# Kernel tuning notes

Measured on AMD Instinct MI355X. Metric: run time of the kernel, lower is better.

The kernel has to match this reference:

```python
import jax, jax.numpy as jnp
import numpy as np

B, C, N = 8, 512, 2048

def setup_inputs() -> dict:
    key = jax.random.key(0)
    ks = jax.random.split(key, 7)
    s = 1.0 / np.sqrt(C)
    return {
        "x": jax.random.normal(ks[0], (B, C, N), dtype=jnp.float32),
        "wq": jax.random.normal(ks[1], (C, C), dtype=jnp.float32) * s,
        "bq": jax.random.normal(ks[2], (C,), dtype=jnp.float32) * s,
        "wk": jax.random.normal(ks[3], (C, C), dtype=jnp.float32) * s,
        "bk": jax.random.normal(ks[4], (C,), dtype=jnp.float32) * s,
        "wv": jax.random.normal(ks[5], (C, C), dtype=jnp.float32) * s,
        "bv": jax.random.normal(ks[6], (C,), dtype=jnp.float32) * s,
    }

def reference(x, wq, bq, wk, bk, wv, bv):
    # Conv1d with kernel=1 == pointwise channel matmul: [B,C,N] -> [B,C,N]
    q = jnp.einsum('oc,bcn->bon', wq, x) + bq[None, :, None]
    k = jnp.einsum('oc,bcn->bon', wk, x) + bk[None, :, None]
    v = jnp.einsum('oc,bcn->bon', wv, x) + bv[None, :, None]
    # scores[b,i,j] = sum_c q[b,c,i] * k[b,c,j]; softmax over j (no scaling, as in source)
    scores = jnp.einsum('bci,bcj->bij', q, k)
    attn = jax.nn.softmax(scores, axis=-1)  # [B,N,N]
    # out[b,c,i] = sum_j v[b,c,j] * attn[b,i,j]
    out = jnp.einsum('bcj,bij->bci', v, attn)
    return out + x
```

## Files before the change

### kernel.cpp

```cpp
#include <hip/hip_runtime.h>
#include <hip/hip_bf16.h>

typedef _Float16 half_t;
typedef _Float16 f16x8 __attribute__((ext_vector_type(8)));
typedef float f32x4 __attribute__((ext_vector_type(4)));

#define AS1 __attribute__((address_space(1)))
#define AS3 __attribute__((address_space(3)))

constexpr int CB = 512;
constexpr int NB = 2048;
constexpr int BB = 8;

__device__ inline f32x4 mfma16(f16x8 a, f16x8 b, f32x4 c) {
  return __builtin_amdgcn_mfma_f32_16x16x32_f16(a, b, c, 0, 0, 0);
}

__device__ inline void xcd_swizzle(int& bx, int& by, int& bz) {
  const int gx = gridDim.x, gy = gridDim.y, gz = gridDim.z;
  const int nwg = gx * gy * gz;
  int lin = blockIdx.x + gx * (blockIdx.y + gy * blockIdx.z);
  if ((nwg & 7) == 0) {
    const int q = nwg >> 3;
    lin = (lin & 7) * q + (lin >> 3);
  }
  bx = lin % gx;
  int tmp = lin / gx;
  by = tmp % gy;
  bz = tmp / gy;
}

__global__ __launch_bounds__(256) void prep_all(
    const float* __restrict__ x, const float* __restrict__ wq,
    const float* __restrict__ wk, const float* __restrict__ wv,
    const float* __restrict__ bq,
    half_t* __restrict__ xh, half_t* __restrict__ xn,
    half_t* __restrict__ wvh, float* __restrict__ u, float* __restrict__ Gp) {
  __shared__ float smem[64 * 68 * 2];
  const int b = blockIdx.x;
  const int t = threadIdx.x;

  if (b < 8192) {
    float (*tile)[33] = (float(*)[33])smem;
    const int bz = b >> 10, by = (b >> 6) & 15, bx = b & 63;
    const int c0 = by * 32, n0 = bx * 32;
    const int tx = t & 31, ty = t >> 5;
    const float* xb = x + (size_t)bz * CB * NB;
    half_t* xnb = xn + (size_t)bz * CB * NB;
#pragma unroll
    for (int r = 0; r < 4; r++) {
      float v = xb[(size_t)(c0 + ty + 8 * r) * NB + n0 + tx];
      tile[ty + 8 * r][tx] = v;
      xnb[(size_t)(c0 + ty + 8 * r) * NB + n0 + tx] = (half_t)v;
    }
    __syncthreads();
    size_t base = (size_t)bz * NB * CB;
#pragma unroll
    for (int r = 0; r < 4; r++)
      xh[base + (size_t)(n0 + ty + 8 * r) * CB + c0 + tx] = (half_t)tile[tx][ty + 8 * r];
  } else if (b < 8704) {
    const int g = b - 8192;
    const int d0 = (g & 7) * 64, c0 = ((g >> 3) & 7) * 64, o0 = (g >> 6) * 64;
    float (*aq)[68] = (float(*)[68])smem;
    float (*ak)[68] = (float(*)[68])(smem + 64 * 68);
    {
      const int r = t >> 2, cbase = (t & 3) * 16;
      const float* q = wq + (size_t)(o0 + r) * CB + c0 + cbase;
      const float* k = wk + (size_t)(o0 + r) * CB + d0 + cbase;
#pragma unroll
      for (int q4 = 0; q4 < 4; q4++) {
        *(float4*)&aq[r][cbase + q4 * 4] = *(const float4*)(q + q4 * 4);
        *(float4*)&ak[r][cbase + q4 * 4] = *(const float4*)(k + q4 * 4);
      }
    }
    __syncthreads();
    const int tc = t & 15, td = t >> 4;
    float acc[4][4] = {};
#pragma unroll 8
    for (int o = 0; o < 64; o++) {
      float4 a4 = *(const float4*)&aq[o][tc * 4];
      float4 b4 = *(const float4*)&ak[o][td * 4];
      float av[4] = {a4.x, a4.y, a4.z, a4.w};
      float bv[4] = {b4.x, b4.y, b4.z, b4.w};
#pragma unroll
      for (int i = 0; i < 4; i++)
#pragma unroll
        for (int j = 0; j < 4; j++)
          acc[i][j] += av[i] * bv[j];
    }
    float* gz = Gp + (size_t)(g >> 6) * CB * CB;
#pragma unroll
    for (int i = 0; i < 4; i++) {
      int c = c0 + tc * 4 + i;
#pragma unroll
      for (int j = 0; j < 4; j++)
        gz[(size_t)c * CB + d0 + td * 4 + j] = acc[i][j];
    }
  } else {
    const int p = b - 8704;
    if (p < 1024) {
      int i = p * 256 + t;
      if (i < CB * CB) wvh[i] = (half_t)wv[i];
    } else {
      int d = (p - 1024) * 256 + t;
      if (d < CB) {
        float s = 0.0f;
        for (int o = 0; o < CB; o++) s += bq[o] * wk[(size_t)o * CB + d];
        u[d] = s;
      }
    }
  }
}

__global__ __launch_bounds__(256) void prep2(
    const float* __restrict__ Gp, half_t* __restrict__ Gh,
    const half_t* __restrict__ xh, const float* __restrict__ u,
    float* __restrict__ ub) {
  const int b = blockIdx.x;
  const int t = threadIdx.x;
  if (b < 1024) {
    int i = b * 256 + t;
    if (i < CB * CB) {
      float s = 0.0f;
#pragma unroll
      for (int z = 0; z < 8; z++) s += Gp[(size_t)z * CB * CB + i];
      Gh[i] = (half_t)s;
    }
  } else {
    __shared__ float us[CB];
    for (int i = t; i < CB; i += 256) us[i] = u[i];
    __syncthreads();
    int row = (b - 1024) * 4 + (t >> 6);
    int lane = t & 63;
    f16x8 vh = *(const f16x8*)(xh + (size_t)row * CB + lane * 8);
    float s = 0.0f;
#pragma unroll
    for (int i = 0; i < 8; i++) s += us[lane * 8 + i] * (float)vh[i];
#pragma unroll
    for (int off = 32; off; off >>= 1) s += __shfl_xor(s, off);
    if (lane == 0) ub[row] = s;
  }
}

template <int BIAS, int EPI, int NT>
__global__ __launch_bounds__(256) void gemm_nt(
    const half_t* __restrict__ A, int lda, long sA,
    const half_t* __restrict__ Bh, int ldb, long sB,
    void* __restrict__ D, int ldd, long sD,
    const float* __restrict__ bias, long sBias,
    const half_t* __restrict__ R, int ldr, long sR) {
  constexpr int TSZ = 128 * 32;
  __shared__ alignas(16) half_t sm[2 * 2 * TSZ];

  int bxi, byi, bzi;
  xcd_swizzle(bxi, byi, bzi);
  const int t = threadIdx.x;
  const int z = bzi;
  const half_t* Ab  = A  + (size_t)z * sA + (size_t)(byi * 128) * lda;
  const half_t* Bbh = Bh + (size_t)z * sB + (size_t)(bxi * 128) * ldb;
  const int wid = t >> 6, l15 = t & 15, hi = (t >> 4) & 3;
  const int wr = wid >> 1, wc = wid & 1;
  const int lineA = t >> 2, eoff = (t & 3) * 8;

  f32x4 acc[4][4] = {};

  auto stage = [&](int buf, int kt) {
    half_t* base = sm + buf * (2 * TSZ);
#pragma unroll
    for (int p = 0; p < 2; p++) {
      size_t goA = (size_t)(p * 64 + lineA) * lda + kt * 32 + eoff;
      size_t goB = (size_t)(p * 64 + lineA) * ldb + kt * 32 + eoff;
      int lo = p * 2048 + t * 8;
      __builtin_amdgcn_global_load_lds((const AS1 void*)(Ab + goA),  (AS3 void*)(base + lo), 16, 0, 0);
      __builtin_amdgcn_global_load_lds((const AS1 void*)(Bbh + goB), (AS3 void*)(base + TSZ + lo), 16, 0, 0);
    }
  };

  stage(0, 0);
  __syncthreads();
  int cur = 0;
  for (int kt = 0; kt < NT; kt++) {
    if (kt + 1 < NT) stage(cur ^ 1, kt + 1);
    const half_t* bb = sm + cur * (2 * TSZ);
    f16x8 af[4], bf[4];
#pragma unroll
    for (int f = 0; f < 4; f++) {
      af[f] = *(const f16x8*)(bb + (wr * 64 + f * 16 + l15) * 32 + hi * 8);
      bf[f] = *(const f16x8*)(bb + TSZ + (wc * 64 + f * 16 + l15) * 32 + hi * 8);
    }
#pragma unroll
    for (int fm = 0; fm < 4; fm++)
#pragma unroll
      for (int fn = 0; fn < 4; fn++)
        acc[fm][fn] = mfma16(af[fm], bf[fn], acc[fm][fn]);
    __syncthreads();
    cur ^= 1;
  }

  const int row0 = byi * 128 + wr * 64;
  const int col0 = bxi * 128 + wc * 64;
#pragma unroll
  for (int fm = 0; fm < 4; fm++) {
    int rowb = row0 + fm * 16 + hi * 4;
#pragma unroll
    for (int fn = 0; fn < 4; fn++) {
      int col = col0 + fn * 16 + l15;
      float bc = (BIAS == 1) ? bias[(size_t)z * sBias + col] : 0.0f;
#pragma unroll
      for (int r = 0; r < 4; r++) {
        float val = acc[fm][fn][r] + bc;
        size_t di = (size_t)(rowb + r) * ldd + col;
        if (EPI == 3) {
          val += (float)R[(size_t)z * sR + (size_t)(rowb + r) * ldr + col];
          ((float*)D)[(size_t)z * sD + di] = val;
        } else {
          float sv = fminf(fmaxf(val * 256.0f, -32767.0f), 32767.0f);
          ((short*)D)[(size_t)z * sD + di] = (short)__float2int_rn(sv);
        }
      }
    }
  }
}

__global__ __launch_bounds__(256) void gemm_vyt(
    const half_t* __restrict__ xh, const half_t* __restrict__ wvh,
    const half_t* __restrict__ Gh, const float* __restrict__ bv,
    half_t* __restrict__ v, half_t* __restrict__ YTh) {
  constexpr int TSZ = 128 * 32;
  __shared__ alignas(16) half_t sm[2 * 2 * TSZ];

  int bxi, byi, bzi;
  xcd_swizzle(bxi, byi, bzi);
  const int t = threadIdx.x;

  const half_t* Ab;
  const half_t* Bb;
  half_t* Dz;
  int ldd, row0b, col0b;
  const float* rowbias = nullptr;
  if (bzi < 8) {
    const int z = bzi;
    Ab = wvh + (size_t)(byi * 128) * CB;
    Bb = xh + (size_t)z * NB * CB + (size_t)(bxi * 128) * CB;
    Dz = v + (size_t)z * CB * NB;
    ldd = NB; row0b = byi * 128; col0b = bxi * 128;
    rowbias = bv;
  } else {
    const int z = bzi - 8;
    const int lin2 = byi * 16 + bxi;
    const int xp = lin2 & 3, yp = lin2 >> 2;
    Ab = xh + (size_t)z * NB * CB + (size_t)(yp * 128) * CB;
    Bb = Gh + (size_t)(xp * 128) * CB;
    Dz = YTh + (size_t)z * NB * CB;
    ldd = CB; row0b = yp * 128; col0b = xp * 128;
  }

  const int wid = t >> 6, l15 = t & 15, hi = (t >> 4) & 3;
  const int wr = wid >> 1, wc = wid & 1;
  const int lineA = t >> 2, eoff = (t & 3) * 8;

  f32x4 acc[4][4] = {};

  auto stage = [&](int buf, int kt) {
    half_t* base = sm + buf * (2 * TSZ);
#pragma unroll
    for (int p = 0; p < 2; p++) {
      size_t go = (size_t)(p * 64 + lineA) * CB + kt * 32 + eoff;
      int lo = p * 2048 + t * 8;
      __builtin_amdgcn_global_load_lds((const AS1 void*)(Ab + go), (AS3 void*)(base + lo), 16, 0, 0);
      __builtin_amdgcn_global_load_lds((const AS1 void*)(Bb + go), (AS3 void*)(base + TSZ + lo), 16, 0, 0);
    }
  };

  stage(0, 0);
  __syncthreads();
  int cur = 0;
  for (int kt = 0; kt < 16; kt++) {
    if (kt + 1 < 16) stage(cur ^ 1, kt + 1);
    const half_t* bb = sm + cur * (2 * TSZ);
    f16x8 af[4], bf[4];
#pragma unroll
    for (int f = 0; f < 4; f++) {
      af[f] = *(const f16x8*)(bb + (wr * 64 + f * 16 + l15) * 32 + hi * 8);
      bf[f] = *(const f16x8*)(bb + TSZ + (wc * 64 + f * 16 + l15) * 32 + hi * 8);
    }
#pragma unroll
    for (int fm = 0; fm < 4; fm++)
#pragma unroll
      for (int fn = 0; fn < 4; fn++)
        acc[fm][fn] = mfma16(af[fm], bf[fn], acc[fm][fn]);
    __syncthreads();
    cur ^= 1;
  }

  const int row0 = row0b + wr * 64;
  const int col0 = col0b + wc * 64;
#pragma unroll
  for (int fm = 0; fm < 4; fm++) {
    int rowb = row0 + fm * 16 + hi * 4;
#pragma unroll
    for (int fn = 0; fn < 4; fn++) {
      int col = col0 + fn * 16 + l15;
#pragma unroll
      for (int r = 0; r < 4; r++) {
        float val = acc[fm][fn][r];
        if (rowbias) val += rowbias[rowb + r];
        Dz[(size_t)(rowb + r) * ldd + col] = (half_t)val;
      }
    }
  }
}

struct alignas(16) H8 { half_t h[8]; };
struct alignas(16) S8 { short s[8]; };

__global__ __launch_bounds__(256) void softmax_rows(const short* __restrict__ S,
                                                    half_t* __restrict__ P) {
  const short* row = S + (size_t)blockIdx.x * NB;
  int t = threadIdx.x;
  S8 r8 = *reinterpret_cast<const S8*>(row + t * 8);
  float vals[8];
#pragma unroll
  for (int i = 0; i < 8; i++) vals[i] = (float)r8.s[i] * 0.00390625f;
  float m = vals[0];
#pragma unroll
  for (int i = 1; i < 8; i++) m = fmaxf(m, vals[i]);
#pragma unroll
  for (int off = 32; off; off >>= 1) m = fmaxf(m, __shfl_xor(m, off));
  __shared__ float redm[4], reds[4];
  if ((t & 63) == 0) redm[t >> 6] = m;
  __syncthreads();
  m = fmaxf(fmaxf(redm[0], redm[1]), fmaxf(redm[2], redm[3]));
  float e[8], s = 0.0f;
#pragma unroll
  for (int i = 0; i < 8; i++) { e[i] = __expf(vals[i] - m); s += e[i]; }
#pragma unroll
  for (int off = 32; off; off >>= 1) s += __shfl_xor(s, off);
  if ((t & 63) == 0) reds[t >> 6] = s;
  __syncthreads();
  s = reds[0] + reds[1] + reds[2] + reds[3];
  float inv = 1.0f / s;
  H8 ob;
#pragma unroll
  for (int i = 0; i < 8; i++) ob.h[i] = (half_t)(e[i] * inv);
  *reinterpret_cast<H8*>(P + (size_t)blockIdx.x * NB + t * 8) = ob;
}

extern "C" void kernel_launch(void* const* d_in, const int* in_sizes, int n_in,
                              void* d_out, int out_size, void* d_ws, size_t ws_size,
                              hipStream_t stream) {
  const float* x  = (const float*)d_in[0];
  const float* wq = (const float*)d_in[1];
  const float* bq = (const float*)d_in[2];
  const float* wk = (const float*)d_in[3];
  const float* wv = (const float*)d_in[5];
  const float* bv = (const float*)d_in[6];
  float* out = (float*)d_out;

  const size_t MB = 1u << 20;
  if (ws_size < 196 * MB) return;

  char* ws = (char*)d_ws;
  half_t* xh   = (half_t*)(ws + 0);
  half_t* YTh  = (half_t*)(ws + 16 * MB);
  half_t* v    = (half_t*)(ws + 32 * MB);
  short*  Ss   = (short*)(ws + 48 * MB);
  float*  Gp   = (float*)(ws + 48 * MB);
  half_t* Pd   = (half_t*)(ws + 112 * MB);
  half_t* xn   = (half_t*)(ws + 176 * MB);
  half_t* Gh   = (half_t*)(ws + 192 * MB);
  half_t* wvh  = (half_t*)(ws + 192 * MB + 512 * 1024);
  float*  u    = (float*)(ws + 193 * MB);
  float*  ub   = (float*)(ws + 193 * MB + 256 * 1024);

  prep_all<<<9730, 256, 0, stream>>>(x, wq, wk, wv, bq, xh, xn, wvh, u, Gp);

  prep2<<<5120, 256, 0, stream>>>(Gp, Gh, xh, u, ub);

  gemm_vyt<<<dim3(16, 4, 16), 256, 0, stream>>>(xh, wvh, Gh, bv, v, YTh);

  gemm_nt<1, 4, 16><<<dim3(16, 16, 8), 256, 0, stream>>>(
      xh, CB, (long)NB * CB,
      YTh, CB, (long)NB * CB,
      Ss, NB, (long)NB * NB, ub, NB, nullptr, 0, 0);

  softmax_rows<<<BB * NB, 256, 0, stream>>>(Ss, Pd);

  gemm_nt<0, 3, 64><<<dim3(16, 4, 8), 256, 0, stream>>>(
      v, NB, (long)CB * NB,
      Pd, NB, (long)NB * NB,
      out, NB, (long)CB * NB, nullptr, 0,
      xn, NB, (long)CB * NB);
}
```

Baseline: 201.8 us.

## Add dedicated 256x256-tile score GEMM with triple-buffered LDS pipeline

```diff
diff --git a/kernel.cpp b/kernel.cpp
--- a/kernel.cpp
+++ b/kernel.cpp
@@ -139,6 +139,117 @@
 #pragma unroll
     for (int off = 32; off; off >>= 1) s += __shfl_xor(s, off);
     if (lane == 0) ub[row] = s;
+  }
+}
+
+__global__ __launch_bounds__(512) void gemm_s256(
+    const half_t* __restrict__ xh, const half_t* __restrict__ YTh,
+    short* __restrict__ Ss, const float* __restrict__ ub) {
+  constexpr int NT = 16;
+  constexpr int BUFE = 16384;
+  __shared__ alignas(16) half_t sm[3 * BUFE];
+
+  int bxi, byi, bzi;
+  xcd_swizzle(bxi, byi, bzi);
+  const int t = threadIdx.x;
+  const int z = bzi;
+  const half_t* Ap = xh  + (size_t)z * NB * CB + (size_t)(byi * 256) * CB;
+  const half_t* Bp = YTh + (size_t)z * NB * CB + (size_t)(bxi * 256) * CB;
+
+  const int wid = t >> 6, wm = wid >> 2, wn = wid & 3;
+  const int l15 = t & 15, hi = (t >> 4) & 3;
+  const int sr = t >> 2, sc = (t & 3) * 8;
+
+  f32x4 acc[8][4] = {};
+
+  auto stageA = [&](int buf, int kt) {
+    half_t* dst = sm + buf * BUFE;
+#pragma unroll
+    for (int i = 0; i < 2; i++)
+      __builtin_amdgcn_global_load_lds(
+          (const AS1 void*)(Ap + (size_t)(i * 128 + sr) * CB + kt * 32 + sc),
+          (AS3 void*)(dst + i * 4096 + t * 8), 16, 0, 0);
+  };
+  auto stageB = [&](int buf, int kt) {
+    half_t* dst = sm + buf * BUFE + 8192;
+#pragma unroll
+    for (int i = 0; i < 2; i++)
+      __builtin_amdgcn_global_load_lds(
+          (const AS1 void*)(Bp + (size_t)(i * 128 + sr) * CB + kt * 32 + sc),
+          (AS3 void*)(dst + i * 4096 + t * 8), 16, 0, 0);
+  };
+
+  stageA(0, 0); stageB(0, 0);
+  stageA(1, 1); stageB(1, 1);
+  asm volatile("s_waitcnt vmcnt(4)" ::: "memory");
+  __builtin_amdgcn_s_barrier();
+  asm volatile("" ::: "memory");
+
+  int rb = 0;
+  for (int kt = 0; kt < NT; kt++) {
+    const half_t* Abuf = sm + rb * BUFE;
+    const half_t* Bbuf = Abuf + 8192;
+    const int sb = (rb + 2 >= 3) ? rb - 1 : rb + 2;
+
+    f16x8 af[8], bf[4];
+#pragma unroll
+    for (int f = 0; f < 4; f++)
+      af[f] = *(const f16x8*)(Abuf + (wm * 128 + f * 16 + l15) * 32 + hi * 8);
+#pragma unroll
+    for (int n = 0; n < 4; n++)
+      bf[n] = *(const f16x8*)(Bbuf + (wn * 64 + n * 16 + l15) * 32 + hi * 8);
+    if (kt + 2 < NT) stageA(sb, kt + 2);
+    __builtin_amdgcn_s_barrier();
+    asm volatile("s_waitcnt lgkmcnt(0)" ::: "memory");
+    __builtin_amdgcn_s_setprio(1);
+#pragma unroll
+    for (int m = 0; m < 4; m++)
+#pragma unroll
+      for (int n = 0; n < 4; n++)
+        acc[m][n] = mfma16(af[m], bf[n], acc[m][n]);
+    __builtin_amdgcn_s_setprio(0);
+    __builtin_amdgcn_s_barrier();
+    asm volatile("" ::: "memory");
+
+#pragma unroll
+    for (int f = 4; f < 8; f++)
+      af[f] = *(const f16x8*)(Abuf + (wm * 128 + f * 16 + l15) * 32 + hi * 8);
+    if (kt + 2 < NT) stageB(sb, kt + 2);
+    __builtin_amdgcn_s_barrier();
+    asm volatile("s_waitcnt lgkmcnt(0)" ::: "memory");
+    __builtin_amdgcn_s_setprio(1);
+#pragma unroll
+    for (int m = 4; m < 8; m++)
+#pragma unroll
+      for (int n = 0; n < 4; n++)
+        acc[m][n] = mfma16(af[m], bf[n], acc[m][n]);
+    __builtin_amdgcn_s_setprio(0);
+    if (kt + 1 < NT) {
+      if (kt + 2 < NT) asm volatile("s_waitcnt vmcnt(4)" ::: "memory");
+      else             asm volatile("s_waitcnt vmcnt(0)" ::: "memory");
+    }
+    __builtin_amdgcn_s_barrier();
+    asm volatile("" ::: "memory");
+    rb = (rb + 1 == 3) ? 0 : rb + 1;
+  }
+
+  const int row0 = byi * 256 + wm * 128;
+  const int col0 = bxi * 256 + wn * 64;
+  short* Sz = Ss + (size_t)z * NB * NB;
+  const float* ubz = ub + (size_t)z * NB;
+#pragma unroll
+  for (int m = 0; m < 8; m++) {
+    int rowb = row0 + m * 16 + hi * 4;
+#pragma unroll
+    for (int n = 0; n < 4; n++) {
+      int col = col0 + n * 16 + l15;
+      float bc = ubz[col];
+#pragma unroll
+      for (int r = 0; r < 4; r++) {
+        float sv = fminf(fmaxf((acc[m][n][r] + bc) * 256.0f, -32767.0f), 32767.0f);
+        Sz[(size_t)(rowb + r) * NB + col] = (short)__float2int_rn(sv);
+      }
+    }
   }
 }
 
@@ -374,15 +485,11 @@
   float*  ub   = (float*)(ws + 193 * MB + 256 * 1024);
 
   prep_all<<<9730, 256, 0, stream>>>(x, wq, wk, wv, bq, xh, xn, wvh, u, Gp);
-
   prep2<<<5120, 256, 0, stream>>>(Gp, Gh, xh, u, ub);
 
   gemm_vyt<<<dim3(16, 4, 16), 256, 0, stream>>>(xh, wvh, Gh, bv, v, YTh);
 
-  gemm_nt<1, 4, 16><<<dim3(16, 16, 8), 256, 0, stream>>>(
-      xh, CB, (long)NB * CB,
-      YTh, CB, (long)NB * CB,
-      Ss, NB, (long)NB * NB, ub, NB, nullptr, 0, 0);
+  gemm_s256<<<dim3(8, 8, 8), 512, 0, stream>>>(xh, YTh, Ss, ub);
 
   softmax_rows<<<BB * NB, 256, 0, stream>>>(Ss, Pd);
 
```

Result: faster. 194.8 us (-3.4%).
